# Optimization experiments

Hardware: AMD Instinct MI355X
Metric: run time of the kernel (lower is better)

The kernel has to match this reference:

```python
import jax, jax.numpy as jnp
import numpy as np

R = 45        # num_dep_rels
L = 384       # sent_len
D = 512       # word representation dim = in_size*2
E_REL = 15    # dep_rel_emb_size
IN4 = 1024    # in_size*4
HOPS = 3
THRESH = 1e-06


def setup_inputs() -> dict:
    key = jax.random.key(0)
    ks = jax.random.split(key, 10)
    energy = jax.random.uniform(ks[0], (1, R, L, L), dtype=jnp.float32)
    word_h = jax.random.normal(ks[1], (1, L, D), dtype=jnp.float32)
    e1 = jax.random.normal(ks[2], (D,), dtype=jnp.float32)
    e2 = jax.random.normal(ks[3], (D,), dtype=jnp.float32)
    # learned params
    rel_embs = jax.random.normal(ks[4], (R, E_REL), dtype=jnp.float32)
    Wc = jax.random.normal(ks[5], (2 * D + E_REL, D), dtype=jnp.float32) * 0.02
    bc = jnp.zeros((D,), dtype=jnp.float32)
    Wk = jax.random.normal(ks[6], (HOPS, IN4, IN4), dtype=jnp.float32) * 0.02
    bk = jnp.zeros((HOPS, IN4), dtype=jnp.float32)
    Wh = jax.random.normal(ks[7], (HOPS, IN4, IN4), dtype=jnp.float32) * 0.02
    bh = jnp.zeros((HOPS, IN4), dtype=jnp.float32)
    return {"energy": energy, "word_h": word_h, "e1": e1, "e2": e2,
            "sent_len": L, "rel_embs": rel_embs, "Wc": Wc, "bc": bc,
            "Wk": Wk, "bk": bk, "Wh": Wh, "bh": bh}


def reference(energy, word_h, e1, e2, sent_len, rel_embs, Wc, bc, Wk, bk, Wh, bh):
    Ls = sent_len
    E = energy[0, :, :Ls, :Ls]                 # [R, L, L]
    marg = E.sum(axis=0)                       # [L, L] marginal energy
    # threshold back-off (try t, t/10, t/100 until some arc survives)
    m0 = marg > THRESH
    m1 = marg > THRESH * 0.1
    m2 = marg > THRESH * 0.01
    mask = jnp.where(m0.any(), m0, jnp.where(m1.any(), m1, m2))  # [L, L]

    H = word_h[0, :Ls]                         # [L, D]
    w = marg.reshape(-1)                       # [L*L] arc weights
    # rel embedding per arc: sum_r E[r,h,d] * rel_embs[r,e]
    rels = jnp.einsum('rhd,re->hde', E, rel_embs).reshape(Ls * Ls, E_REL)
    head_t = jnp.repeat(H, Ls, axis=0) * w[:, None]   # [L*L, D]
    dep_t = jnp.tile(H, (Ls, 1)) * w[:, None]         # [L*L, D]
    arc_in = jnp.concatenate([head_t, rels, dep_t], axis=1)  # [L*L, 2D+15]
    mem_bank = jax.nn.leaky_relu(arc_in @ Wc + bc)    # [L*L, D] (dropout=eval)
    maskf = mask.reshape(-1)                          # [L*L]

    # multi-hop memory attention; filtered-out arcs get zero attention weight
    inputs = jnp.concatenate([e1, e2])                # [1024]
    for i in range(HOPS):
        kv = inputs @ Wk[i] + bk[i]                   # [1024]
        k_, v_ = jnp.split(kv, 2)                     # chunk along dim 0
        k_ = jnp.tanh(k_)
        v_ = jax.nn.leaky_relu(v_)
        scores = jnp.where(maskf, mem_bank @ k_, -1e30)  # [L*L]
        dist = jax.nn.softmax(scores)
        mem_rep = dist @ mem_bank                     # [D]
        inputs = jax.nn.leaky_relu(jnp.concatenate([v_, mem_rep]) @ Wh[i] + bh[i])
    return inputs
```

## Files before the change

### kernel.cpp

```cpp
#include <hip/hip_runtime.h>
#include <hip/hip_bf16.h>
#include <cstdint>
#include <cstddef>

#define LL      147456
#define NBLK    768
#define CHB     12

typedef __attribute__((ext_vector_type(8))) short  short8;
typedef __attribute__((ext_vector_type(4))) float  f32x4;

#define EPACK_OFF   0u
#define MARG_OFF    14155776u
#define A_OFF       14745600u
#define BT_OFF      15532032u
#define UTGP_OFF    16318464u
#define XIN_OFF     16367696u
#define KBUF_OFF    16371792u
#define VBUF_OFF    16373840u
#define XVEC_OFF    16375888u
#define PM_OFF      16379984u
#define PL_OFF      16383056u
#define PACC_OFF    16386128u
#define SRAW_OFF    17958992u
#define BLKF_OFF    18548816u

#define SKIP_LD     30.0f

static __device__ __forceinline__ ushort f2bf(float x) {
  uint u = __float_as_uint(x);
  return (ushort)((u + 0x7fffu + ((u >> 16) & 1u)) >> 16);
}
static __device__ __forceinline__ float lrelu(float x) { return fmaxf(x, 0.01f * x); }

__global__ __launch_bounds__(256) void k_prep(
    const float* __restrict__ E, uint4* __restrict__ ep,
    float* __restrict__ marg, int* __restrict__ blkflags,
    const float* __restrict__ H, const float* __restrict__ Wc,
    const float* __restrict__ rel, const float* __restrict__ bc,
    float* __restrict__ A, float* __restrict__ Btp, uint4* __restrict__ Utgp) {
  __shared__ float Hs[8][512];
  __shared__ float Ps[8][512];
  __shared__ int fsh;
  int b = blockIdx.x, t = threadIdx.x;
  if (b < 576) {
    if (t == 0) fsh = 0;
    size_t hd = (size_t)b * 256 + t;
    float ev[48];
#pragma unroll
    for (int r = 0; r < 45; ++r) ev[r] = E[(size_t)r * LL + hd];
    ev[45] = 1.0f; ev[46] = 0.f; ev[47] = 0.f;
    float s = 0.f;
#pragma unroll
    for (int r = 0; r < 45; ++r) s += ev[r];
#pragma unroll
    for (int o = 0; o < 6; ++o) {
      uint w[4];
#pragma unroll
      for (int p = 0; p < 4; ++p)
        w[p] = (uint)f2bf(ev[8 * o + 2 * p]) | ((uint)f2bf(ev[8 * o + 2 * p + 1]) << 16);
      uint4 v; v.x = w[0]; v.y = w[1]; v.z = w[2]; v.w = w[3];
      ep[(size_t)o * LL + hd] = v;
    }
    marg[hd] = s;
    int f = (s > 1e-6f ? 1 : 0) | (s > 1e-7f ? 2 : 0) | (s > 1e-8f ? 4 : 0);
#pragma unroll
    for (int d = 1; d < 64; d <<= 1) f |= __shfl_xor(f, d);
    __syncthreads();
    if ((t & 63) == 0) atomicOr(&fsh, f);
    __syncthreads();
    if (t == 0) blkflags[b] = fsh;
  } else {
    int bb = b - 576;
    if (bb < 96) {
      bool roleA = (bb < 48);
      int g0 = (roleA ? bb : bb - 48) * 8;
      const float* Wcp = Wc + (size_t)(roleA ? 0 : 527) * 512;
      float* dst = roleA ? A : Btp;
      for (int i = t; i < 8 * 512; i += 256) Hs[i >> 9][i & 511] = H[(size_t)g0 * 512 + i];
      __syncthreads();
      int cq = t & 127, q = t >> 7;
      int c0 = cq * 4;
      f32x4 acc[8];
#pragma unroll
      for (int i = 0; i < 8; ++i) acc[i] = (f32x4){0.f, 0.f, 0.f, 0.f};
      for (int k = q * 256; k < q * 256 + 256; ++k) {
        f32x4 wv = *(const f32x4*)&Wcp[(size_t)k * 512 + c0];
#pragma unroll
        for (int i = 0; i < 8; ++i) { float hv = Hs[i][k]; acc[i] += hv * wv; }
      }
      if (q == 1) {
#pragma unroll
        for (int i = 0; i < 8; ++i) *(f32x4*)&Ps[i][c0] = acc[i];
      }
      __syncthreads();
      if (q == 0) {
#pragma unroll
        for (int i = 0; i < 8; ++i) {
          acc[i] += *(const f32x4*)&Ps[i][c0];
          *(f32x4*)&dst[(size_t)(g0 + i) * 512 + c0] = acc[i];
        }
      }
    } else {
      for (int c = t; c < 512; c += 256) {
        float uv[48];
#pragma unroll
        for (int k = 0; k < 45; ++k) {
          float s = 0.f;
#pragma unroll
          for (int e = 0; e < 15; ++e) s += rel[k * 15 + e] * Wc[(size_t)(512 + e) * 512 + c];
          uv[k] = s;
        }
        uv[45] = bc[c]; uv[46] = 0.f; uv[47] = 0.f;
#pragma unroll
        for (int g = 0; g < 6; ++g) {
          uint w[4];
#pragma unroll
          for (int p = 0; p < 4; ++p)
            w[p] = (uint)f2bf(uv[g * 8 + 2 * p]) | ((uint)f2bf(uv[g * 8 + 2 * p + 1]) << 16);
          uint4 v; v.x = w[0]; v.y = w[1]; v.z = w[2]; v.w = w[3];
          Utgp[g * 512 + c] = v;
        }
      }
    }
  }
}

__global__ __launch_bounds__(256) void k_gemv(const float* __restrict__ W, const float* __restrict__ bias,
                                              const float* __restrict__ xA, const float* __restrict__ xB,
                                              float* __restrict__ outA,
                                              float* __restrict__ outB, float* __restrict__ out2, int mode) {
  __shared__ float xs[1024];
  __shared__ float red[8][32];
  int t = threadIdx.x;
  for (int i = t; i < 1024; i += 256) xs[i] = (i < 512) ? xA[i] : xB[i - 512];
  __syncthreads();
  int jj = t & 31, kq = t >> 5;
  int j = blockIdx.x * 32 + jj;
  float acc = 0.f;
#pragma unroll 8
  for (int k = kq * 128; k < kq * 128 + 128; ++k) acc = fmaf(xs[k], W[(size_t)k * 1024 + j], acc);
  red[kq][jj] = acc;
  __syncthreads();
  if (kq == 0) {
    float s = bias[j];
#pragma unroll
    for (int q = 0; q < 8; ++q) s += red[q][jj];
    if (mode == 0) {
      if (j < 512) outA[j] = tanhf(s);
      else outB[j - 512] = lrelu(s);
    } else {
      float rv = lrelu(s);
      outA[j] = rv;
      if (out2) out2[j] = rv;
    }
  }
}

__global__ __launch_bounds__(256, 3) void k_scores(
    const uint4* __restrict__ ep, const float* __restrict__ marg,
    const float* __restrict__ A, const float* __restrict__ Btp,
    const uint4* __restrict__ Utgp, const int* __restrict__ blkflags,
    const float* __restrict__ kvec,
    float* __restrict__ pm, float* __restrict__ pl, float* __restrict__ sraw) {
  __shared__ __align__(16) uint4 uthF[6 * 512];
  __shared__ float sbuf[CHB * 16];
  __shared__ float redw[8];
  __shared__ int fsh;
  int t = threadIdx.x, b = blockIdx.x;
  int dbt = b >> 5, hg = b & 31;
  int dbase = dbt * 16, h0 = hg * CHB;
  int lane = t & 63, wid = t >> 6;
  int l15 = lane & 15, qq = lane >> 4;

  if (t == 0) fsh = 0;
  for (int i = t; i < 6 * 512; i += 256) uthF[i] = Utgp[i];
  int f = 0;
  for (int i = t; i < 576; i += 256) f |= blkflags[i];
#pragma unroll
  for (int d = 1; d < 64; d <<= 1) f |= __shfl_xor(f, d);

  const short8 zero8 = (short8){0, 0, 0, 0, 0, 0, 0, 0};
  short8 a0[3], a1[3];
  f32x4 wq[3];
#pragma unroll
  for (int k3 = 0; k3 < 3; ++k3) {
    int h = h0 + wid * 3 + k3;
    int hda = h * 384 + dbase + l15;
    uint4 r0 = ep[(size_t)qq * LL + hda];
    a0[k3] = *(short8*)&r0;
    if (qq < 2) { uint4 r1 = ep[(size_t)(4 + qq) * LL + hda]; a1[k3] = *(short8*)&r1; }
    else a1[k3] = zero8;
    wq[k3] = *(const f32x4*)&marg[h * 384 + dbase + qq * 4];
  }
  __syncthreads();
  if ((t & 63) == 0) atomicOr(&fsh, f);

  float sp[3][4];
#pragma unroll
  for (int k3 = 0; k3 < 3; ++k3)
#pragma unroll
    for (int j = 0; j < 4; ++j) sp[k3][j] = 0.f;

  for (int half = 0; half < 2; ++half) {
#pragma unroll 4
    for (int tt = 0; tt < 16; ++tt) {
      int c = half * 256 + tt * 16 + l15;
      short8 b0 = *(short8*)&uthF[qq * 512 + c];
      short8 b1 = (qq < 2) ? *(short8*)&uthF[(4 + qq) * 512 + c] : zero8;
      const float* Bp = &Btp[(size_t)(dbase + qq * 4) * 512 + c];
      float bt0 = Bp[0], bt1 = Bp[512], bt2 = Bp[1024], bt3 = Bp[1536];
      const float* Ap = &A[(size_t)(h0 + wid * 3) * 512 + c];
      float av[3]; av[0] = Ap[0]; av[1] = Ap[512]; av[2] = Ap[1024];
      float kv = kvec[c];
#pragma unroll
      for (int k3 = 0; k3 < 3; ++k3) {
        f32x4 cc = (f32x4){0.f, 0.f, 0.f, 0.f};
        cc = __builtin_amdgcn_mfma_f32_16x16x32_bf16(a0[k3], b0, cc, 0, 0, 0);
        cc = __builtin_amdgcn_mfma_f32_16x16x32_bf16(a1[k3], b1, cc, 0, 0, 0);
        float aw = av[k3];
        float x0 = cc[0] + wq[k3][0] * (aw + bt0); float mb0 = fmaxf(x0, 0.01f * x0);
        float x1 = cc[1] + wq[k3][1] * (aw + bt1); float mb1 = fmaxf(x1, 0.01f * x1);
        float x2 = cc[2] + wq[k3][2] * (aw + bt2); float mb2 = fmaxf(x2, 0.01f * x2);
        float x3 = cc[3] + wq[k3][3] * (aw + bt3); float mb3 = fmaxf(x3, 0.01f * x3);
        sp[k3][0] = fmaf(mb0, kv, sp[k3][0]);
        sp[k3][1] = fmaf(mb1, kv, sp[k3][1]);
        sp[k3][2] = fmaf(mb2, kv, sp[k3][2]);
        sp[k3][3] = fmaf(mb3, kv, sp[k3][3]);
      }
    }
  }
#pragma unroll
  for (int k3 = 0; k3 < 3; ++k3)
#pragma unroll
    for (int j = 0; j < 4; ++j) {
#pragma unroll
      for (int d = 1; d < 16; d <<= 1) sp[k3][j] += __shfl_xor(sp[k3][j], d);
    }
  __syncthreads();
  float thr = (fsh & 1) ? 1e-6f : ((fsh & 2) ? 1e-7f : 1e-8f);
  if (l15 == 0) {
#pragma unroll
    for (int k3 = 0; k3 < 3; ++k3) {
      int base = (wid * 3 + k3) * 16 + qq * 4;
#pragma unroll
      for (int j = 0; j < 4; ++j)
        sbuf[base + j] = (wq[k3][j] > thr) ? sp[k3][j] : -1e30f;
    }
  }
  __syncthreads();
  float s = (t < CHB * 16) ? sbuf[t] : -1e30f;
  float m = s;
#pragma unroll
  for (int d = 1; d < 64; d <<= 1) m = fmaxf(m, __shfl_xor(m, d));
  if (lane == 0) redw[wid] = m;
  __syncthreads();
  float mloc = fmaxf(fmaxf(redw[0], redw[1]), fmaxf(redw[2], redw[3]));
  float e = (t < CHB * 16) ? __expf(s - mloc) : 0.f;
#pragma unroll
  for (int d = 1; d < 64; d <<= 1) e += __shfl_xor(e, d);
  if (lane == 0) redw[4 + wid] = e;
  if (t < CHB * 16) sraw[(size_t)b * 192 + t] = s;
  __syncthreads();
  if (t == 0) { pm[b] = mloc; pl[b] = redw[4] + redw[5] + redw[6] + redw[7]; }
}

__global__ __launch_bounds__(256, 3) void k_pv(
    const uint4* __restrict__ ep, const float* __restrict__ marg,
    const float* __restrict__ A, const float* __restrict__ Btp,
    const uint4* __restrict__ Utgp, const float* __restrict__ pm,
    const float* __restrict__ sraw, float* __restrict__ pacc) {
  __shared__ __align__(16) uint4 uthF[6 * 512];
  __shared__ float pbuf[CHB * 16];
  __shared__ float paccs[256];
  __shared__ float redm[4];
  int t = threadIdx.x, b = blockIdx.x;
  int lane = t & 63, wid = t >> 6;

  float m = -1e30f;
  for (int i = t; i < NBLK; i += 256) m = fmaxf(m, pm[i]);
#pragma unroll
  for (int d = 1; d < 64; d <<= 1) m = fmaxf(m, __shfl_xor(m, d));
  if (lane == 0) redm[wid] = m;
  __syncthreads();
  float M = fmaxf(fmaxf(redm[0], redm[1]), fmaxf(redm[2], redm[3]));
  float pmb = pm[b];
  if (pmb - M < -SKIP_LD) return;

  int dbt = b >> 5, hg = b & 31;
  int dbase = dbt * 16, h0 = hg * CHB;
  int l15 = lane & 15, qq = lane >> 4;

  for (int i = t; i < 6 * 512; i += 256) uthF[i] = Utgp[i];
  if (t < CHB * 16) pbuf[t] = __expf(sraw[(size_t)b * 192 + t] - pmb);

  const short8 zero8 = (short8){0, 0, 0, 0, 0, 0, 0, 0};
  short8 a0[3], a1[3];
  f32x4 wq[3];
#pragma unroll
  for (int k3 = 0; k3 < 3; ++k3) {
    int h = h0 + wid * 3 + k3;
    int hda = h * 384 + dbase + l15;
    uint4 r0 = ep[(size_t)qq * LL + hda];
    a0[k3] = *(short8*)&r0;
    if (qq < 2) { uint4 r1 = ep[(size_t)(4 + qq) * LL + hda]; a1[k3] = *(short8*)&r1; }
    else a1[k3] = zero8;
    wq[k3] = *(const f32x4*)&marg[h * 384 + dbase + qq * 4];
  }
  __syncthreads();

  float pvw[3][4];
#pragma unroll
  for (int k3 = 0; k3 < 3; ++k3)
#pragma unroll
    for (int j = 0; j < 4; ++j)
      pvw[k3][j] = pbuf[(wid * 3 + k3) * 16 + qq * 4 + j];

  for (int half = 0; half < 2; ++half) {
    paccs[t] = 0.f;
    __syncthreads();
#pragma unroll 4
    for (int tt = 0; tt < 16; ++tt) {
      int c = half * 256 + tt * 16 + l15;
      short8 b0 = *(short8*)&uthF[qq * 512 + c];
      short8 b1 = (qq < 2) ? *(short8*)&uthF[(4 + qq) * 512 + c] : zero8;
      const float* Bp = &Btp[(size_t)(dbase + qq * 4) * 512 + c];
      float bt0 = Bp[0], bt1 = Bp[512], bt2 = Bp[1024], bt3 = Bp[1536];
      const float* Ap = &A[(size_t)(h0 + wid * 3) * 512 + c];
      float av[3]; av[0] = Ap[0]; av[1] = Ap[512]; av[2] = Ap[1024];
      float acc_t = 0.f;
#pragma unroll
      for (int k3 = 0; k3 < 3; ++k3) {
        f32x4 cc = (f32x4){0.f, 0.f, 0.f, 0.f};
        cc = __builtin_amdgcn_mfma_f32_16x16x32_bf16(a0[k3], b0, cc, 0, 0, 0);
        cc = __builtin_amdgcn_mfma_f32_16x16x32_bf16(a1[k3], b1, cc, 0, 0, 0);
        float aw = av[k3];
        float x0 = cc[0] + wq[k3][0] * (aw + bt0); float mb0 = fmaxf(x0, 0.01f * x0);
        float x1 = cc[1] + wq[k3][1] * (aw + bt1); float mb1 = fmaxf(x1, 0.01f * x1);
        float x2 = cc[2] + wq[k3][2] * (aw + bt2); float mb2 = fmaxf(x2, 0.01f * x2);
        float x3 = cc[3] + wq[k3][3] * (aw + bt3); float mb3 = fmaxf(x3, 0.01f * x3);
        acc_t = fmaf(pvw[k3][0], mb0, fmaf(pvw[k3][1], mb1,
                fmaf(pvw[k3][2], mb2, fmaf(pvw[k3][3], mb3, acc_t))));
      }
      acc_t += __shfl_xor(acc_t, 16);
      acc_t += __shfl_xor(acc_t, 32);
      if (lane < 16) atomicAdd(&paccs[tt * 16 + l15], acc_t);
    }
    __syncthreads();
    pacc[(size_t)b * 512 + half * 256 + t] = paccs[t];
    __syncthreads();
  }
}

__global__ __launch_bounds__(256) void k_combine(const float* __restrict__ pm,
                                                 const float* __restrict__ pl,
                                                 const float* __restrict__ pacc,
                                                 const float* __restrict__ vbuf,
                                                 float* __restrict__ xvec) {
  __shared__ float sc[NBLK];
  __shared__ float red[256];
  __shared__ float red2[16][17];
  int t = threadIdx.x;
  float m = -1e30f;
  for (int i = t; i < NBLK; i += 256) m = fmaxf(m, pm[i]);
  red[t] = m;
  __syncthreads();
  for (int s = 128; s > 0; s >>= 1) { if (t < s) red[t] = fmaxf(red[t], red[t + s]); __syncthreads(); }
  float M = red[0];
  __syncthreads();
  float ls = 0.f;
  for (int i = t; i < NBLK; i += 256) {
    float d = pm[i] - M;
    float e = (d < -SKIP_LD) ? 0.f : __expf(d);
    sc[i] = e;
    ls += e * pl[i];
  }
  red[t] = ls;
  __syncthreads();
  for (int s = 128; s > 0; s >>= 1) { if (t < s) red[t] += red[t + s]; __syncthreads(); }
  float L = red[0];
  __syncthreads();
  int cl = t & 15, bg = t >> 4;
  int c = blockIdx.x * 16 + cl;
  float s = 0.f;
  for (int bb = bg * (NBLK / 16); bb < (bg + 1) * (NBLK / 16); ++bb) {
    float w = sc[bb];
    if (w > 0.f) s += pacc[(size_t)bb * 512 + c] * w;
  }
  red2[bg][cl] = s;
  __syncthreads();
  if (bg == 0) {
    float tot = 0.f;
#pragma unroll
    for (int i = 0; i < 16; ++i) tot += red2[i][cl];
    xvec[512 + c] = tot / L;
    xvec[c] = vbuf[c];
  }
}

extern "C" void kernel_launch(void* const* d_in, const int* in_sizes, int n_in,
                              void* d_out, int out_size, void* d_ws, size_t ws_size,
                              hipStream_t stream) {
  const float* E   = (const float*)d_in[0];
  const float* H   = (const float*)d_in[1];
  const float* e1  = (const float*)d_in[2];
  const float* e2  = (const float*)d_in[3];
  const float* rel = (const float*)d_in[5];
  const float* Wc  = (const float*)d_in[6];
  const float* bc  = (const float*)d_in[7];
  const float* Wk  = (const float*)d_in[8];
  const float* bk  = (const float*)d_in[9];
  const float* Wh  = (const float*)d_in[10];
  const float* bh  = (const float*)d_in[11];

  char* ws = (char*)d_ws;
  uint4*  ep     = (uint4*)(ws + EPACK_OFF);
  float*  marg   = (float*)(ws + MARG_OFF);
  float*  Abuf   = (float*)(ws + A_OFF);
  float*  Btp    = (float*)(ws + BT_OFF);
  uint4*  Utgp   = (uint4*)(ws + UTGP_OFF);
  float*  xin    = (float*)(ws + XIN_OFF);
  float*  kbuf   = (float*)(ws + KBUF_OFF);
  float*  vbuf   = (float*)(ws + VBUF_OFF);
  float*  xvec   = (float*)(ws + XVEC_OFF);
  float*  pm     = (float*)(ws + PM_OFF);
  float*  pl     = (float*)(ws + PL_OFF);
  float*  pacc   = (float*)(ws + PACC_OFF);
  float*  sraw   = (float*)(ws + SRAW_OFF);
  int*    blkf   = (int*)(ws + BLKF_OFF);

  k_prep<<<673, 256, 0, stream>>>(E, ep, marg, blkf, H, Wc, rel, bc, Abuf, Btp, Utgp);

  for (int hop = 0; hop < 3; ++hop) {
    const float* Wki = Wk + (size_t)hop * 1024 * 1024;
    const float* bki = bk + (size_t)hop * 1024;
    const float* Whi = Wh + (size_t)hop * 1024 * 1024;
    const float* bhi = bh + (size_t)hop * 1024;
    k_gemv<<<32, 256, 0, stream>>>(Wki, bki, hop == 0 ? e1 : xin,
                                   hop == 0 ? e2 : xin + 512, kbuf, vbuf, (float*)nullptr, 0);
    k_scores<<<NBLK, 256, 0, stream>>>(ep, marg, Abuf, Btp, Utgp, blkf, kbuf, pm, pl, sraw);
    k_pv<<<NBLK, 256, 0, stream>>>(ep, marg, Abuf, Btp, Utgp, pm, sraw, pacc);
    k_combine<<<32, 256, 0, stream>>>(pm, pl, pacc, vbuf, xvec);
    k_gemv<<<32, 256, 0, stream>>>(Whi, bhi, xvec, xvec + 512, xin, (float*)nullptr,
                                   hop == 2 ? (float*)d_out : (float*)nullptr, 1);
  }
}
```

Before: 229.5 us.

## Fuse softmax combine into output GEMV and rebalance prep kernel

Merges the combine kernel into the Wh GEMV, so each of the 32 blocks redundantly computes the softmax normaliser and the full 512-wide weighted memory vector. Surviving partial blocks are compacted with a ballot into a list. This removes one launch per hop and the xvec round trip through global memory, at the cost of every block re-reading pacc. The prep kernel now has each thread handle two arcs with float2 loads and uses smaller H tiles for the A/B GEMMs, which changes the block count. k_scores preloads the k vector into registers per half.

```diff
diff --git a/kernel.cpp b/kernel.cpp
--- a/kernel.cpp
+++ b/kernel.cpp
@@ -6,6 +6,7 @@
 #define LL      147456
 #define NBLK    768
 #define CHB     12
+#define NPACK   288
 
 typedef __attribute__((ext_vector_type(8))) short  short8;
 typedef __attribute__((ext_vector_type(4))) float  f32x4;
@@ -18,7 +19,6 @@
 #define XIN_OFF     16367696u
 #define KBUF_OFF    16371792u
 #define VBUF_OFF    16373840u
-#define XVEC_OFF    16375888u
 #define PM_OFF      16379984u
 #define PL_OFF      16383056u
 #define PACC_OFF    16386128u
@@ -39,97 +39,102 @@
     const float* __restrict__ H, const float* __restrict__ Wc,
     const float* __restrict__ rel, const float* __restrict__ bc,
     float* __restrict__ A, float* __restrict__ Btp, uint4* __restrict__ Utgp) {
-  __shared__ float Hs[8][512];
-  __shared__ float Ps[8][512];
+  __shared__ float Hs[4][512];
+  __shared__ float Ps[4][512];
   __shared__ int fsh;
   int b = blockIdx.x, t = threadIdx.x;
-  if (b < 576) {
+  if (b < 192) {
+    bool roleA = (b < 96);
+    int g0 = (roleA ? b : b - 96) * 4;
+    const float* Wcp = Wc + (size_t)(roleA ? 0 : 527) * 512;
+    float* dst = roleA ? A : Btp;
+    for (int i = t; i < 4 * 512; i += 256) Hs[i >> 9][i & 511] = H[(size_t)g0 * 512 + i];
+    __syncthreads();
+    int cq = t & 127, q = t >> 7;
+    int c0 = cq * 4;
+    f32x4 acc[4];
+#pragma unroll
+    for (int i = 0; i < 4; ++i) acc[i] = (f32x4){0.f, 0.f, 0.f, 0.f};
+    for (int k = q * 256; k < q * 256 + 256; ++k) {
+      f32x4 wv = *(const f32x4*)&Wcp[(size_t)k * 512 + c0];
+#pragma unroll
+      for (int i = 0; i < 4; ++i) { float hv = Hs[i][k]; acc[i] += hv * wv; }
+    }
+    if (q == 1) {
+#pragma unroll
+      for (int i = 0; i < 4; ++i) *(f32x4*)&Ps[i][c0] = acc[i];
+    }
+    __syncthreads();
+    if (q == 0) {
+#pragma unroll
+      for (int i = 0; i < 4; ++i) {
+        acc[i] += *(const f32x4*)&Ps[i][c0];
+        *(f32x4*)&dst[(size_t)(g0 + i) * 512 + c0] = acc[i];
+      }
+    }
+  } else if (b == 192) {
+    for (int c = t; c < 512; c += 256) {
+      float uv[48];
+#pragma unroll
+      for (int k = 0; k < 45; ++k) {
+        float s = 0.f;
+#pragma unroll
+        for (int e = 0; e < 15; ++e) s += rel[k * 15 + e] * Wc[(size_t)(512 + e) * 512 + c];
+        uv[k] = s;
+      }
+      uv[45] = bc[c]; uv[46] = 0.f; uv[47] = 0.f;
+#pragma unroll
+      for (int g = 0; g < 6; ++g) {
+        uint w[4];
+#pragma unroll
+        for (int p = 0; p < 4; ++p)
+          w[p] = (uint)f2bf(uv[g * 8 + 2 * p]) | ((uint)f2bf(uv[g * 8 + 2 * p + 1]) << 16);
+        uint4 v; v.x = w[0]; v.y = w[1]; v.z = w[2]; v.w = w[3];
+        Utgp[g * 512 + c] = v;
+      }
+    }
+  } else {
     if (t == 0) fsh = 0;
-    size_t hd = (size_t)b * 256 + t;
-    float ev[48];
-#pragma unroll
-    for (int r = 0; r < 45; ++r) ev[r] = E[(size_t)r * LL + hd];
-    ev[45] = 1.0f; ev[46] = 0.f; ev[47] = 0.f;
-    float s = 0.f;
-#pragma unroll
-    for (int r = 0; r < 45; ++r) s += ev[r];
+    int bp = b - 193;
+    size_t hd0 = (size_t)bp * 512 + 2 * t;
+    float2 ev[46];
+#pragma unroll
+    for (int r = 0; r < 45; ++r) ev[r] = *(const float2*)&E[(size_t)r * LL + hd0];
+    ev[45] = make_float2(1.0f, 1.0f);
+    float s0 = 0.f, s1 = 0.f;
+#pragma unroll
+    for (int r = 0; r < 45; ++r) { s0 += ev[r].x; s1 += ev[r].y; }
 #pragma unroll
     for (int o = 0; o < 6; ++o) {
-      uint w[4];
-#pragma unroll
-      for (int p = 0; p < 4; ++p)
-        w[p] = (uint)f2bf(ev[8 * o + 2 * p]) | ((uint)f2bf(ev[8 * o + 2 * p + 1]) << 16);
-      uint4 v; v.x = w[0]; v.y = w[1]; v.z = w[2]; v.w = w[3];
-      ep[(size_t)o * LL + hd] = v;
-    }
-    marg[hd] = s;
-    int f = (s > 1e-6f ? 1 : 0) | (s > 1e-7f ? 2 : 0) | (s > 1e-8f ? 4 : 0);
+      uint wa[4], wb[4];
+#pragma unroll
+      for (int p = 0; p < 4; ++p) {
+        int r0 = 8 * o + 2 * p, r1 = r0 + 1;
+        float a0 = (r0 < 46) ? ev[r0].x : 0.f, a1 = (r1 < 46) ? ev[r1].x : 0.f;
+        float b0 = (r0 < 46) ? ev[r0].y : 0.f, b1 = (r1 < 46) ? ev[r1].y : 0.f;
+        wa[p] = (uint)f2bf(a0) | ((uint)f2bf(a1) << 16);
+        wb[p] = (uint)f2bf(b0) | ((uint)f2bf(b1) << 16);
+      }
+      uint4 va; va.x = wa[0]; va.y = wa[1]; va.z = wa[2]; va.w = wa[3];
+      uint4 vb; vb.x = wb[0]; vb.y = wb[1]; vb.z = wb[2]; vb.w = wb[3];
+      ep[(size_t)o * LL + hd0] = va;
+      ep[(size_t)o * LL + hd0 + 1] = vb;
+    }
+    *(float2*)&marg[hd0] = make_float2(s0, s1);
+    int f = (s0 > 1e-6f ? 1 : 0) | (s0 > 1e-7f ? 2 : 0) | (s0 > 1e-8f ? 4 : 0)
+          | (s1 > 1e-6f ? 1 : 0) | (s1 > 1e-7f ? 2 : 0) | (s1 > 1e-8f ? 4 : 0);
 #pragma unroll
     for (int d = 1; d < 64; d <<= 1) f |= __shfl_xor(f, d);
     __syncthreads();
     if ((t & 63) == 0) atomicOr(&fsh, f);
     __syncthreads();
-    if (t == 0) blkflags[b] = fsh;
-  } else {
-    int bb = b - 576;
-    if (bb < 96) {
-      bool roleA = (bb < 48);
-      int g0 = (roleA ? bb : bb - 48) * 8;
-      const float* Wcp = Wc + (size_t)(roleA ? 0 : 527) * 512;
-      float* dst = roleA ? A : Btp;
-      for (int i = t; i < 8 * 512; i += 256) Hs[i >> 9][i & 511] = H[(size_t)g0 * 512 + i];
-      __syncthreads();
-      int cq = t & 127, q = t >> 7;
-      int c0 = cq * 4;
-      f32x4 acc[8];
-#pragma unroll
-      for (int i = 0; i < 8; ++i) acc[i] = (f32x4){0.f, 0.f, 0.f, 0.f};
-      for (int k = q * 256; k < q * 256 + 256; ++k) {
-        f32x4 wv = *(const f32x4*)&Wcp[(size_t)k * 512 + c0];
-#pragma unroll
-        for (int i = 0; i < 8; ++i) { float hv = Hs[i][k]; acc[i] += hv * wv; }
-      }
-      if (q == 1) {
-#pragma unroll
-        for (int i = 0; i < 8; ++i) *(f32x4*)&Ps[i][c0] = acc[i];
-      }
-      __syncthreads();
-      if (q == 0) {
-#pragma unroll
-        for (int i = 0; i < 8; ++i) {
-          acc[i] += *(const f32x4*)&Ps[i][c0];
-          *(f32x4*)&dst[(size_t)(g0 + i) * 512 + c0] = acc[i];
-        }
-      }
-    } else {
-      for (int c = t; c < 512; c += 256) {
-        float uv[48];
-#pragma unroll
-        for (int k = 0; k < 45; ++k) {
-          float s = 0.f;
-#pragma unroll
-          for (int e = 0; e < 15; ++e) s += rel[k * 15 + e] * Wc[(size_t)(512 + e) * 512 + c];
-          uv[k] = s;
-        }
-        uv[45] = bc[c]; uv[46] = 0.f; uv[47] = 0.f;
-#pragma unroll
-        for (int g = 0; g < 6; ++g) {
-          uint w[4];
-#pragma unroll
-          for (int p = 0; p < 4; ++p)
-            w[p] = (uint)f2bf(uv[g * 8 + 2 * p]) | ((uint)f2bf(uv[g * 8 + 2 * p + 1]) << 16);
-          uint4 v; v.x = w[0]; v.y = w[1]; v.z = w[2]; v.w = w[3];
-          Utgp[g * 512 + c] = v;
-        }
-      }
-    }
+    if (t == 0) blkflags[bp] = fsh;
   }
 }
 
 __global__ __launch_bounds__(256) void k_gemv(const float* __restrict__ W, const float* __restrict__ bias,
                                               const float* __restrict__ xA, const float* __restrict__ xB,
-                                              float* __restrict__ outA,
-                                              float* __restrict__ outB, float* __restrict__ out2, int mode) {
+                                              float* __restrict__ outA, float* __restrict__ outB) {
   __shared__ float xs[1024];
   __shared__ float red[8][32];
   int t = threadIdx.x;
@@ -146,14 +151,8 @@
     float s = bias[j];
 #pragma unroll
     for (int q = 0; q < 8; ++q) s += red[q][jj];
-    if (mode == 0) {
-      if (j < 512) outA[j] = tanhf(s);
-      else outB[j - 512] = lrelu(s);
-    } else {
-      float rv = lrelu(s);
-      outA[j] = rv;
-      if (out2) out2[j] = rv;
-    }
+    if (j < 512) outA[j] = tanhf(s);
+    else outB[j - 512] = lrelu(s);
   }
 }
 
@@ -176,7 +175,7 @@
   if (t == 0) fsh = 0;
   for (int i = t; i < 6 * 512; i += 256) uthF[i] = Utgp[i];
   int f = 0;
-  for (int i = t; i < 576; i += 256) f |= blkflags[i];
+  for (int i = t; i < NPACK; i += 256) f |= blkflags[i];
 #pragma unroll
   for (int d = 1; d < 64; d <<= 1) f |= __shfl_xor(f, d);
 
@@ -203,6 +202,9 @@
     for (int j = 0; j < 4; ++j) sp[k3][j] = 0.f;
 
   for (int half = 0; half < 2; ++half) {
+    float kreg[16];
+#pragma unroll
+    for (int tt = 0; tt < 16; ++tt) kreg[tt] = kvec[half * 256 + tt * 16 + l15];
 #pragma unroll 4
     for (int tt = 0; tt < 16; ++tt) {
       int c = half * 256 + tt * 16 + l15;
@@ -212,7 +214,6 @@
       float bt0 = Bp[0], bt1 = Bp[512], bt2 = Bp[1024], bt3 = Bp[1536];
       const float* Ap = &A[(size_t)(h0 + wid * 3) * 512 + c];
       float av[3]; av[0] = Ap[0]; av[1] = Ap[512]; av[2] = Ap[1024];
-      float kv = kvec[c];
 #pragma unroll
       for (int k3 = 0; k3 < 3; ++k3) {
         f32x4 cc = (f32x4){0.f, 0.f, 0.f, 0.f};
@@ -223,10 +224,10 @@
         float x1 = cc[1] + wq[k3][1] * (aw + bt1); float mb1 = fmaxf(x1, 0.01f * x1);
         float x2 = cc[2] + wq[k3][2] * (aw + bt2); float mb2 = fmaxf(x2, 0.01f * x2);
         float x3 = cc[3] + wq[k3][3] * (aw + bt3); float mb3 = fmaxf(x3, 0.01f * x3);
-        sp[k3][0] = fmaf(mb0, kv, sp[k3][0]);
-        sp[k3][1] = fmaf(mb1, kv, sp[k3][1]);
-        sp[k3][2] = fmaf(mb2, kv, sp[k3][2]);
-        sp[k3][3] = fmaf(mb3, kv, sp[k3][3]);
+        sp[k3][0] = fmaf(mb0, kreg[tt], sp[k3][0]);
+        sp[k3][1] = fmaf(mb1, kreg[tt], sp[k3][1]);
+        sp[k3][2] = fmaf(mb2, kreg[tt], sp[k3][2]);
+        sp[k3][3] = fmaf(mb3, kreg[tt], sp[k3][3]);
       }
     }
   }
@@ -352,22 +353,27 @@
   }
 }
 
-__global__ __launch_bounds__(256) void k_combine(const float* __restrict__ pm,
-                                                 const float* __restrict__ pl,
-                                                 const float* __restrict__ pacc,
-                                                 const float* __restrict__ vbuf,
-                                                 float* __restrict__ xvec) {
+__global__ __launch_bounds__(256) void k_gemvc(
+    const float* __restrict__ W, const float* __restrict__ bias,
+    const float* __restrict__ vbuf, const float* __restrict__ pm,
+    const float* __restrict__ pl, const float* __restrict__ pacc,
+    float* __restrict__ outA, float* __restrict__ out2) {
+  __shared__ float xs[1024];
   __shared__ float sc[NBLK];
-  __shared__ float red[256];
-  __shared__ float red2[16][17];
+  __shared__ int slist[NBLK];
+  __shared__ int scnt_sh;
+  __shared__ float redm[8];
+  __shared__ float red[8][32];
   int t = threadIdx.x;
+  int lane = t & 63, wid = t >> 6;
+
   float m = -1e30f;
   for (int i = t; i < NBLK; i += 256) m = fmaxf(m, pm[i]);
-  red[t] = m;
-  __syncthreads();
-  for (int s = 128; s > 0; s >>= 1) { if (t < s) red[t] = fmaxf(red[t], red[t + s]); __syncthreads(); }
-  float M = red[0];
-  __syncthreads();
+#pragma unroll
+  for (int d = 1; d < 64; d <<= 1) m = fmaxf(m, __shfl_xor(m, d));
+  if (lane == 0) redm[wid] = m;
+  __syncthreads();
+  float M = fmaxf(fmaxf(redm[0], redm[1]), fmaxf(redm[2], redm[3]));
   float ls = 0.f;
   for (int i = t; i < NBLK; i += 256) {
     float d = pm[i] - M;
@@ -375,26 +381,54 @@
     sc[i] = e;
     ls += e * pl[i];
   }
-  red[t] = ls;
-  __syncthreads();
-  for (int s = 128; s > 0; s >>= 1) { if (t < s) red[t] += red[t + s]; __syncthreads(); }
-  float L = red[0];
-  __syncthreads();
-  int cl = t & 15, bg = t >> 4;
-  int c = blockIdx.x * 16 + cl;
-  float s = 0.f;
-  for (int bb = bg * (NBLK / 16); bb < (bg + 1) * (NBLK / 16); ++bb) {
-    float w = sc[bb];
-    if (w > 0.f) s += pacc[(size_t)bb * 512 + c] * w;
-  }
-  red2[bg][cl] = s;
-  __syncthreads();
-  if (bg == 0) {
-    float tot = 0.f;
-#pragma unroll
-    for (int i = 0; i < 16; ++i) tot += red2[i][cl];
-    xvec[512 + c] = tot / L;
-    xvec[c] = vbuf[c];
+#pragma unroll
+  for (int d = 1; d < 64; d <<= 1) ls += __shfl_xor(ls, d);
+  if (lane == 0) redm[4 + wid] = ls;
+  __syncthreads();
+  float L = redm[4] + redm[5] + redm[6] + redm[7];
+
+  if (wid == 0) {
+    int cnt = 0;
+#pragma unroll
+    for (int rnd = 0; rnd < NBLK / 64; ++rnd) {
+      int bb = rnd * 64 + lane;
+      bool p = sc[bb] > 0.f;
+      unsigned long long mask = __ballot(p);
+      int off = __popcll(mask & ((1ull << lane) - 1ull));
+      if (p) slist[cnt + off] = bb;
+      cnt += __popcll(mask);
+    }
+    if (lane == 0) scnt_sh = cnt;
+  }
+  __syncthreads();
+  int S = scnt_sh;
+  for (int c = t; c < 512; c += 256) xs[c] = vbuf[c];
+#pragma unroll
+  for (int half = 0; half < 2; ++half) {
+    int c = t + half * 256;
+    float s = 0.f;
+    for (int k = 0; k < S; ++k) {
+      int bb = slist[k];
+      s += pacc[(size_t)bb * 512 + c] * sc[bb];
+    }
+    xs[512 + c] = s / L;
+  }
+  __syncthreads();
+
+  int jj = t & 31, kq = t >> 5;
+  int j = blockIdx.x * 32 + jj;
+  float acc = 0.f;
+#pragma unroll 8
+  for (int k = kq * 128; k < kq * 128 + 128; ++k) acc = fmaf(xs[k], W[(size_t)k * 1024 + j], acc);
+  red[kq][jj] = acc;
+  __syncthreads();
+  if (kq == 0) {
+    float s = bias[j];
+#pragma unroll
+    for (int q = 0; q < 8; ++q) s += red[q][jj];
+    float rv = lrelu(s);
+    outA[j] = rv;
+    if (out2) out2[j] = rv;
   }
 }
 
@@ -422,14 +456,13 @@
   float*  xin    = (float*)(ws + XIN_OFF);
   float*  kbuf   = (float*)(ws + KBUF_OFF);
   float*  vbuf   = (float*)(ws + VBUF_OFF);
-  float*  xvec   = (float*)(ws + XVEC_OFF);
   float*  pm     = (float*)(ws + PM_OFF);
   float*  pl     = (float*)(ws + PL_OFF);
   float*  pacc   = (float*)(ws + PACC_OFF);
   float*  sraw   = (float*)(ws + SRAW_OFF);
   int*    blkf   = (int*)(ws + BLKF_OFF);
 
-  k_prep<<<673, 256, 0, stream>>>(E, ep, marg, blkf, H, Wc, rel, bc, Abuf, Btp, Utgp);
+  k_prep<<<481, 256, 0, stream>>>(E, ep, marg, blkf, H, Wc, rel, bc, Abuf, Btp, Utgp);
 
   for (int hop = 0; hop < 3; ++hop) {
     const float* Wki = Wk + (size_t)hop * 1024 * 1024;
@@ -437,11 +470,10 @@
     const float* Whi = Wh + (size_t)hop * 1024 * 1024;
     const float* bhi = bh + (size_t)hop * 1024;
     k_gemv<<<32, 256, 0, stream>>>(Wki, bki, hop == 0 ? e1 : xin,
-                                   hop == 0 ? e2 : xin + 512, kbuf, vbuf, (float*)nullptr, 0);
+                                   hop == 0 ? e2 : xin + 512, kbuf, vbuf);
     k_scores<<<NBLK, 256, 0, stream>>>(ep, marg, Abuf, Btp, Utgp, blkf, kbuf, pm, pl, sraw);
     k_pv<<<NBLK, 256, 0, stream>>>(ep, marg, Abuf, Btp, Utgp, pm, sraw, pacc);
-    k_combine<<<32, 256, 0, stream>>>(pm, pl, pacc, vbuf, xvec);
-    k_gemv<<<32, 256, 0, stream>>>(Whi, bhi, xvec, xvec + 512, xin, (float*)nullptr,
-                                   hop == 2 ? (float*)d_out : (float*)nullptr, 1);
-  }
-}
+    k_gemvc<<<32, 256, 0, stream>>>(Whi, bhi, vbuf, pm, pl, pacc, xin,
+                                    hop == 2 ? (float*)d_out : (float*)nullptr);
+  }
+}
```

New measurement: 207.8 us. 9.5% less time.
